# Performance work log

Measured on AMD Instinct MI355X. Metric: run time of the kernel, lower is better.

## Reference

```python
import jax, jax.numpy as jnp
import numpy as np

B, S, D, H = 1, 512, 128, 128
EPS = 1e-5


def layernorm(x, g, b):
    mu = jnp.mean(x, axis=-1, keepdims=True)
    var = jnp.mean(jnp.square(x - mu), axis=-1, keepdims=True)
    return (x - mu) * jax.lax.rsqrt(var + EPS) * g + b


def setup_inputs() -> dict:
    key = jax.random.key(0)
    ks = jax.random.split(key, 10)
    scale_d = 1.0 / np.sqrt(D)
    scale_h = 1.0 / np.sqrt(H)
    return {
        "x": jax.random.normal(ks[0], (B, S, S, D), dtype=jnp.float32),
        "mask": jax.random.uniform(ks[1], (B, S, S), dtype=jnp.float32),
        "norm_g": jnp.ones((D,), jnp.float32),
        "norm_b": jnp.zeros((D,), jnp.float32),
        "Wl": jax.random.normal(ks[2], (H, D), jnp.float32) * scale_d,
        "Wr": jax.random.normal(ks[3], (H, D), jnp.float32) * scale_d,
        "Wlg": jax.random.normal(ks[4], (H, D), jnp.float32) * scale_d,
        "Wrg": jax.random.normal(ks[5], (H, D), jnp.float32) * scale_d,
        "Wog": jax.random.normal(ks[6], (H, D), jnp.float32) * scale_d,
        "out_norm_g": jnp.ones((H,), jnp.float32),
        "out_norm_b": jnp.zeros((H,), jnp.float32),
        "Wout": jax.random.normal(ks[7], (D, H), jnp.float32) * scale_h,
    }


def reference(x, mask, norm_g, norm_b, Wl, Wr, Wlg, Wrg, Wog, out_norm_g, out_norm_b, Wout):
    # x: [B,S,S,D], mask: [B,S,S]
    xn = layernorm(x, norm_g, norm_b)
    m = mask[..., None]  # [B,S,S,1]
    left = (xn @ Wl.T) * m * jax.nn.sigmoid(xn @ Wlg.T)   # [B,S,S,H]
    right = (xn @ Wr.T) * m * jax.nn.sigmoid(xn @ Wrg.T)  # [B,S,S,H]
    out_gate = jax.nn.sigmoid(xn @ Wog.T)                  # [B,S,S,H]
    # per-channel triangular contraction over k
    out = jnp.einsum('bikd,bjkd->bijd', left, right)       # [B,S,S,H]
    out = layernorm(out, out_norm_g, out_norm_b) * out_gate
    return out @ Wout.T  # [B,S,S,D]
```

## Files before the change

kernel.cpp:

```cpp
#include <hip/hip_runtime.h>
#include <hip/hip_bf16.h>
#include <cstdint>

typedef unsigned short u16;
typedef unsigned int   u32;
typedef __bf16 bf16x8 __attribute__((ext_vector_type(8)));
typedef float  f32x4  __attribute__((ext_vector_type(4)));

#define S_    512
#define D_    128
#define H_    128
#define NPOS_ (S_ * S_)
#define LN_EPS 1e-5f

__device__ __forceinline__ u16 f2bf(float f) {
  union { __hip_bfloat16 h; u16 u; } cv;
  cv.h = __float2bfloat16(f);
  return cv.u;
}
__device__ __forceinline__ float bflo(u32 p) { return __uint_as_float(p << 16); }
__device__ __forceinline__ float bfhi(u32 p) { return __uint_as_float(p & 0xffff0000u); }
__device__ __forceinline__ float sigmoidf_(float x) { return 1.f / (1.f + __expf(-x)); }

__device__ __forceinline__ void gld16(const void* g, void* l) {
  __builtin_amdgcn_global_load_lds(
      (const __attribute__((address_space(1))) void*)g,
      (__attribute__((address_space(3))) void*)l, 16, 0, 0);
}

template <int CPR, int TOTAL>
__device__ __forceinline__ void stage_tile(const char* gbase, int ld_bytes, char* lds, int tid) {
#pragma unroll
  for (int c = tid; c < TOTAL; c += 256) {
    int row = c / CPR;
    int col = c - row * CPR;
    gld16(gbase + (size_t)row * ld_bytes + (size_t)col * 16, lds + (size_t)c * 16);
  }
}

__global__ __launch_bounds__(256) void k_prep(
    const float* __restrict__ wl, const float* __restrict__ wlg,
    const float* __restrict__ wr, const float* __restrict__ wrg,
    const float* __restrict__ wog, const float* __restrict__ wout,
    u16* __restrict__ wb) {
  int i = blockIdx.x * 256 + threadIdx.x;
  int m = i >> 14, o = i & 16383;
  const float* src = (m == 0) ? wl : (m == 1) ? wlg : (m == 2) ? wr
                   : (m == 3) ? wrg : (m == 4) ? wog : wout;
  wb[i] = f2bf(src[o]);
}

__global__ __launch_bounds__(256) void k_ln(
    const float* __restrict__ x, const float* __restrict__ ng,
    const float* __restrict__ nb, u32* __restrict__ xn) {
  const int l  = threadIdx.x & 63;
  const int wid = (blockIdx.x * 256 + threadIdx.x) >> 6;
  const int nw  = (gridDim.x * 256) >> 6;
  const float2 gg = ((const float2*)ng)[l];
  const float2 bb = ((const float2*)nb)[l];
  for (int row = wid; row < NPOS_; row += nw) {
    float2 v = ((const float2*)(x + (size_t)row * D_))[l];
    float s = v.x + v.y;
    float q = v.x * v.x + v.y * v.y;
#pragma unroll
    for (int off = 32; off >= 1; off >>= 1) {
      s += __shfl_xor(s, off);
      q += __shfl_xor(q, off);
    }
    float mu  = s * (1.f / 128.f);
    float var = q * (1.f / 128.f) - mu * mu;
    float rs  = rsqrtf(var + LN_EPS);
    float a = (v.x - mu) * rs * gg.x + bb.x;
    float b = (v.y - mu) * rs * gg.y + bb.y;
    xn[(size_t)row * 64 + l] = (u32)f2bf(a) | ((u32)f2bf(b) << 16);
  }
}

__global__ __launch_bounds__(256, 2) void k_proj(
    const u16* __restrict__ xn, const float* __restrict__ mask,
    const u16* __restrict__ wb, u16* __restrict__ left_t,
    u16* __restrict__ right_t, u16* __restrict__ gate_t) {
  __shared__ u16 Bs[128 * 64];
  __shared__ u16 As0[128 * 64];
  __shared__ u16 As1[128 * 64];
  const int g   = blockIdx.y;
  const int r0  = blockIdx.x * 128;
  const int tid = threadIdx.x;
  const int w = tid >> 6, l = tid & 63;
  const int wr = w >> 1, wc = w & 1;
  const u16* W0 = wb + (size_t)((g == 2) ? 4 : 2 * g) * (H_ * D_);
  const u16* W1 = wb + (size_t)(2 * g + 1) * (H_ * D_);

  const f32x4 vz = {0.f, 0.f, 0.f, 0.f};
  f32x4 acc0[4][4], acc1[4][4];
#pragma unroll
  for (int i = 0; i < 4; ++i)
#pragma unroll
    for (int j = 0; j < 4; ++j) { acc0[i][j] = vz; acc1[i][j] = vz; }

#pragma unroll
  for (int kt = 0; kt < 2; ++kt) {
    stage_tile<8, 1024>((const char*)xn + ((size_t)r0 * D_ + kt * 64) * 2, D_ * 2, (char*)Bs, tid);
    stage_tile<8, 1024>((const char*)W0 + (size_t)(kt * 64) * 2, D_ * 2, (char*)As0, tid);
    if (g < 2)
      stage_tile<8, 1024>((const char*)W1 + (size_t)(kt * 64) * 2, D_ * 2, (char*)As1, tid);
    __syncthreads();
#pragma unroll
    for (int kk = 0; kk < 2; ++kk) {
      const int ko = kk * 32 + (l >> 4) * 8;
      bf16x8 bfr[4], a0[4], a1[4];
#pragma unroll
      for (int ni = 0; ni < 4; ++ni)
        bfr[ni] = *(const bf16x8*)&Bs[(wc * 64 + ni * 16 + (l & 15)) * 64 + ko];
#pragma unroll
      for (int mi = 0; mi < 4; ++mi)
        a0[mi] = *(const bf16x8*)&As0[(wr * 64 + mi * 16 + (l & 15)) * 64 + ko];
      if (g < 2) {
#pragma unroll
        for (int mi = 0; mi < 4; ++mi)
          a1[mi] = *(const bf16x8*)&As1[(wr * 64 + mi * 16 + (l & 15)) * 64 + ko];
      }
#pragma unroll
      for (int mi = 0; mi < 4; ++mi)
#pragma unroll
        for (int ni = 0; ni < 4; ++ni) {
          acc0[mi][ni] = __builtin_amdgcn_mfma_f32_16x16x32_bf16(a0[mi], bfr[ni], acc0[mi][ni], 0, 0, 0);
          if (g < 2)
            acc1[mi][ni] = __builtin_amdgcn_mfma_f32_16x16x32_bf16(a1[mi], bfr[ni], acc1[mi][ni], 0, 0, 0);
        }
    }
    __syncthreads();
  }

  const int quad = l >> 4, lc = l & 15;
  u16* dst = (g == 0) ? left_t : (g == 1) ? right_t : gate_t;
#pragma unroll
  for (int ni = 0; ni < 4; ++ni) {
    const int r = r0 + wc * 64 + ni * 16 + lc;
    const float mk = (g < 2) ? mask[r] : 0.f;
#pragma unroll
    for (int mi = 0; mi < 4; ++mi) {
#pragma unroll
      for (int reg = 0; reg < 4; ++reg) {
        const int hrow = wr * 64 + mi * 16 + quad * 4 + reg;
        float v0 = acc0[mi][ni][reg];
        float o;
        if (g < 2) o = v0 * mk * sigmoidf_(acc1[mi][ni][reg]);
        else       o = sigmoidf_(v0);
        dst[(size_t)hrow * NPOS_ + r] = f2bf(o);
      }
    }
  }
}

__global__ __launch_bounds__(256, 2) void k_einsum(
    const u16* __restrict__ left_t, const u16* __restrict__ right_t,
    u16* __restrict__ out_t) {
  const int d = blockIdx.x;
  const int t = blockIdx.y;
  const int i0 = (t >> 2) * 128, j0 = (t & 3) * 128;
  __shared__ u16 As[128 * 64], Bs[128 * 64];
  const u16* L = left_t + (size_t)d * NPOS_;
  const u16* R = right_t + (size_t)d * NPOS_;
  const int tid = threadIdx.x;
  const int w = tid >> 6, l = tid & 63;
  const int wr = w >> 1, wc = w & 1;

  const f32x4 vz = {0.f, 0.f, 0.f, 0.f};
  f32x4 acc[4][4];
#pragma unroll
  for (int i = 0; i < 4; ++i)
#pragma unroll
    for (int j = 0; j < 4; ++j) acc[i][j] = vz;

  for (int kt = 0; kt < 8; ++kt) {
    stage_tile<8, 1024>((const char*)L + ((size_t)i0 * S_ + kt * 64) * 2, S_ * 2, (char*)As, tid);
    stage_tile<8, 1024>((const char*)R + ((size_t)j0 * S_ + kt * 64) * 2, S_ * 2, (char*)Bs, tid);
    __syncthreads();
#pragma unroll
    for (int kk = 0; kk < 2; ++kk) {
      const int ko = kk * 32 + (l >> 4) * 8;
      bf16x8 a[4], b[4];
#pragma unroll
      for (int mi = 0; mi < 4; ++mi)
        a[mi] = *(const bf16x8*)&As[(wr * 64 + mi * 16 + (l & 15)) * 64 + ko];
#pragma unroll
      for (int ni = 0; ni < 4; ++ni)
        b[ni] = *(const bf16x8*)&Bs[(wc * 64 + ni * 16 + (l & 15)) * 64 + ko];
#pragma unroll
      for (int mi = 0; mi < 4; ++mi)
#pragma unroll
        for (int ni = 0; ni < 4; ++ni)
          acc[mi][ni] = __builtin_amdgcn_mfma_f32_16x16x32_bf16(a[mi], b[ni], acc[mi][ni], 0, 0, 0);
    }
    __syncthreads();
  }

  const int quad = l >> 4, lc = l & 15;
  u16* O = out_t + (size_t)d * NPOS_;
#pragma unroll
  for (int mi = 0; mi < 4; ++mi)
#pragma unroll
    for (int ni = 0; ni < 4; ++ni) {
      const int col = j0 + wc * 64 + ni * 16 + lc;
#pragma unroll
      for (int reg = 0; reg < 4; ++reg) {
        const int row = i0 + wr * 64 + mi * 16 + quad * 4 + reg;
        O[(size_t)row * S_ + col] = f2bf(acc[mi][ni][reg]);
      }
    }
}

__global__ __launch_bounds__(256, 2) void k_final(
    const u16* __restrict__ out_t, const u16* __restrict__ gate_t,
    const float* __restrict__ og, const float* __restrict__ ob,
    const u16* __restrict__ wout_b, float* __restrict__ out) {
  __shared__ u16 A_lds[128 * 136];
  __shared__ u16 Wlds[128 * 128];
  __shared__ float psum[4][128], pq[4][128];
  __shared__ float mu_s[128], rs_s[128];
  const int tid = threadIdx.x, w = tid >> 6, l = tid & 63;
  const int r0 = blockIdx.x * 128;

  stage_tile<16, 2048>((const char*)wout_b, 256, (char*)Wlds, tid);

  float s0 = 0.f, s1 = 0.f, q0 = 0.f, q1 = 0.f;
  for (int it = 0; it < 32; ++it) {
    int d = it * 4 + w;
    u32 p = *(const u32*)&out_t[(size_t)d * NPOS_ + r0 + 2 * l];
    float f0 = bflo(p), f1 = bfhi(p);
    s0 += f0; s1 += f1; q0 += f0 * f0; q1 += f1 * f1;
  }
  psum[w][2 * l] = s0; psum[w][2 * l + 1] = s1;
  pq[w][2 * l] = q0;   pq[w][2 * l + 1] = q1;
  __syncthreads();
  if (tid < 128) {
    float s = psum[0][tid] + psum[1][tid] + psum[2][tid] + psum[3][tid];
    float q = pq[0][tid] + pq[1][tid] + pq[2][tid] + pq[3][tid];
    float mu  = s * (1.f / 128.f);
    float var = q * (1.f / 128.f) - mu * mu;
    mu_s[tid] = mu;
    rs_s[tid] = rsqrtf(var + LN_EPS);
  }
  __syncthreads();

  for (int it = 0; it < 32; ++it) {
    int d = it * 4 + w;
    u32 p  = *(const u32*)&out_t[(size_t)d * NPOS_ + r0 + 2 * l];
    u32 gp = *(const u32*)&gate_t[(size_t)d * NPOS_ + r0 + 2 * l];
    float gd = og[d], bd = ob[d];
    float f0 = bflo(p), f1 = bfhi(p);
    float g0 = bflo(gp), g1 = bfhi(gp);
    int ja = 2 * l, jb = 2 * l + 1;
    float a0 = ((f0 - mu_s[ja]) * rs_s[ja] * gd + bd) * g0;
    float a1 = ((f1 - mu_s[jb]) * rs_s[jb] * gd + bd) * g1;
    A_lds[(size_t)ja * 136 + d] = f2bf(a0);
    A_lds[(size_t)jb * 136 + d] = f2bf(a1);
  }
  __syncthreads();

  const int wr = w >> 1, wc = w & 1;
  const f32x4 vz = {0.f, 0.f, 0.f, 0.f};
  f32x4 acc[4][4];
#pragma unroll
  for (int i = 0; i < 4; ++i)
#pragma unroll
    for (int j = 0; j < 4; ++j) acc[i][j] = vz;
#pragma unroll
  for (int kk = 0; kk < 4; ++kk) {
    const int ko = kk * 32 + (l >> 4) * 8;
    bf16x8 a[4], b[4];
#pragma unroll
    for (int mi = 0; mi < 4; ++mi)
      a[mi] = *(const bf16x8*)&A_lds[(wr * 64 + mi * 16 + (l & 15)) * 136 + ko];
#pragma unroll
    for (int ni = 0; ni < 4; ++ni)
      b[ni] = *(const bf16x8*)&Wlds[(wc * 64 + ni * 16 + (l & 15)) * 128 + ko];
#pragma unroll
    for (int mi = 0; mi < 4; ++mi)
#pragma unroll
      for (int ni = 0; ni < 4; ++ni)
        acc[mi][ni] = __builtin_amdgcn_mfma_f32_16x16x32_bf16(a[mi], b[ni], acc[mi][ni], 0, 0, 0);
  }
  const int quad = l >> 4, lc = l & 15;
#pragma unroll
  for (int mi = 0; mi < 4; ++mi)
#pragma unroll
    for (int ni = 0; ni < 4; ++ni) {
      const int dout = wc * 64 + ni * 16 + lc;
#pragma unroll
      for (int reg = 0; reg < 4; ++reg) {
        const int row = r0 + wr * 64 + mi * 16 + quad * 4 + reg;
        out[(size_t)row * D_ + dout] = acc[mi][ni][reg];
      }
    }
}

extern "C" void kernel_launch(void* const* d_in, const int* in_sizes, int n_in,
                              void* d_out, int out_size, void* d_ws, size_t ws_size,
                              hipStream_t stream) {
  const float* x    = (const float*)d_in[0];
  const float* mask = (const float*)d_in[1];
  const float* ng   = (const float*)d_in[2];
  const float* nb   = (const float*)d_in[3];
  const float* Wl   = (const float*)d_in[4];
  const float* Wr   = (const float*)d_in[5];
  const float* Wlg  = (const float*)d_in[6];
  const float* Wrg  = (const float*)d_in[7];
  const float* Wog  = (const float*)d_in[8];
  const float* og   = (const float*)d_in[9];
  const float* ob   = (const float*)d_in[10];
  const float* Wout = (const float*)d_in[11];
  float* out = (float*)d_out;

  const size_t SLAB = (size_t)NPOS_ * H_ * 2;
  char* ws = (char*)d_ws;
  u16* xn      = (u16*)(ws);
  u16* left_t  = (u16*)(ws + SLAB);
  u16* right_t = (u16*)(ws + 2 * SLAB);
  u16* gate_t  = (u16*)(ws + 3 * SLAB);
  u16* wb      = (u16*)(ws + 4 * SLAB);
  u16* out_t   = xn;
  if (ws_size < 4 * SLAB + 6 * H_ * D_ * sizeof(u16)) return;

  k_prep<<<384, 256, 0, stream>>>(Wl, Wlg, Wr, Wrg, Wog, Wout, wb);
  k_ln<<<2048, 256, 0, stream>>>(x, ng, nb, (u32*)xn);
  k_proj<<<dim3(2048, 3), 256, 0, stream>>>(xn, mask, wb, left_t, right_t, gate_t);
  k_einsum<<<dim3(128, 16), 256, 0, stream>>>(left_t, right_t, out_t);
  k_final<<<2048, 256, 0, stream>>>(out_t, gate_t, og, ob, wb + 5 * H_ * D_, out);
}
```

Baseline: 496.8 us.

## Fuse input layernorm into projection kernel with swizzled LDS tile

Merges the layernorm and projection kernels. Each block normalizes its 128 rows straight into an XOR-swizzled LDS tile and then computes all five projections from that tile, instead of three separate blocks each re-reading a bf16 xn buffer. Weight fragments are now read directly from global memory (L2-cached) rather than staged into LDS. This removes the xn round-trip through HBM, one kernel launch, and the triple reload of activations. In exchange each block does more serial work and relies on cached global loads for the weights.

```diff
diff --git a/kernel.cpp b/kernel.cpp
--- a/kernel.cpp
+++ b/kernel.cpp
@@ -50,106 +50,122 @@
   wb[i] = f2bf(src[o]);
 }
 
-__global__ __launch_bounds__(256) void k_ln(
-    const float* __restrict__ x, const float* __restrict__ ng,
-    const float* __restrict__ nb, u32* __restrict__ xn) {
-  const int l  = threadIdx.x & 63;
-  const int wid = (blockIdx.x * 256 + threadIdx.x) >> 6;
-  const int nw  = (gridDim.x * 256) >> 6;
-  const float2 gg = ((const float2*)ng)[l];
-  const float2 bb = ((const float2*)nb)[l];
-  for (int row = wid; row < NPOS_; row += nw) {
-    float2 v = ((const float2*)(x + (size_t)row * D_))[l];
-    float s = v.x + v.y;
-    float q = v.x * v.x + v.y * v.y;
-#pragma unroll
-    for (int off = 32; off >= 1; off >>= 1) {
-      s += __shfl_xor(s, off);
-      q += __shfl_xor(q, off);
-    }
-    float mu  = s * (1.f / 128.f);
-    float var = q * (1.f / 128.f) - mu * mu;
-    float rs  = rsqrtf(var + LN_EPS);
-    float a = (v.x - mu) * rs * gg.x + bb.x;
-    float b = (v.y - mu) * rs * gg.y + bb.y;
-    xn[(size_t)row * 64 + l] = (u32)f2bf(a) | ((u32)f2bf(b) << 16);
-  }
-}
-
-__global__ __launch_bounds__(256, 2) void k_proj(
-    const u16* __restrict__ xn, const float* __restrict__ mask,
+__device__ __forceinline__ void proj_k128(
+    const u16* __restrict__ Wm, const u16* __restrict__ Wg,
+    const u16* Xs, int wr, int wc, int quad, int lq,
+    f32x4 acc0[4][4], f32x4 acc1[4][4]) {
+#pragma unroll
+  for (int ks = 0; ks < 4; ++ks) {
+    const int kc = ks * 4 + quad;
+    bf16x8 b[4], am[4], ag[4];
+#pragma unroll
+    for (int ni = 0; ni < 4; ++ni) {
+      const int br = wc * 64 + ni * 16 + lq;
+      b[ni] = *(const bf16x8*)((const char*)Xs + br * 256 + ((kc ^ (br & 15)) << 4));
+    }
+#pragma unroll
+    for (int mi = 0; mi < 4; ++mi) {
+      const int ar = wr * 64 + mi * 16 + lq;
+      am[mi] = *(const bf16x8*)&Wm[(size_t)ar * D_ + kc * 8];
+      if (Wg) ag[mi] = *(const bf16x8*)&Wg[(size_t)ar * D_ + kc * 8];
+    }
+#pragma unroll
+    for (int mi = 0; mi < 4; ++mi)
+#pragma unroll
+      for (int ni = 0; ni < 4; ++ni) {
+        acc0[mi][ni] = __builtin_amdgcn_mfma_f32_16x16x32_bf16(am[mi], b[ni], acc0[mi][ni], 0, 0, 0);
+        if (Wg)
+          acc1[mi][ni] = __builtin_amdgcn_mfma_f32_16x16x32_bf16(ag[mi], b[ni], acc1[mi][ni], 0, 0, 0);
+      }
+  }
+}
+
+__global__ __launch_bounds__(256, 2) void k_lnproj(
+    const float* __restrict__ x, const float* __restrict__ mask,
+    const float* __restrict__ ng, const float* __restrict__ nb,
     const u16* __restrict__ wb, u16* __restrict__ left_t,
     u16* __restrict__ right_t, u16* __restrict__ gate_t) {
-  __shared__ u16 Bs[128 * 64];
-  __shared__ u16 As0[128 * 64];
-  __shared__ u16 As1[128 * 64];
-  const int g   = blockIdx.y;
-  const int r0  = blockIdx.x * 128;
-  const int tid = threadIdx.x;
-  const int w = tid >> 6, l = tid & 63;
-  const int wr = w >> 1, wc = w & 1;
-  const u16* W0 = wb + (size_t)((g == 2) ? 4 : 2 * g) * (H_ * D_);
-  const u16* W1 = wb + (size_t)(2 * g + 1) * (H_ * D_);
-
+  __shared__ u16 Xs[128 * 128];
+  const int tid = threadIdx.x, w = tid >> 6, l = tid & 63;
+  const int r0 = blockIdx.x * 128;
+  const int half = l >> 5, lh = l & 31;
+
+  {
+    const float4 gg = ((const float4*)ng)[lh];
+    const float4 bb = ((const float4*)nb)[lh];
+#pragma unroll 4
+    for (int it = 0; it < 16; ++it) {
+      const int rr = it * 8 + w * 2 + half;
+      float4 v = ((const float4*)(x + (size_t)(r0 + rr) * D_))[lh];
+      float s = v.x + v.y + v.z + v.w;
+      float q = v.x * v.x + v.y * v.y + v.z * v.z + v.w * v.w;
+#pragma unroll
+      for (int off = 16; off >= 1; off >>= 1) {
+        s += __shfl_xor(s, off);
+        q += __shfl_xor(q, off);
+      }
+      const float mu  = s * (1.f / 128.f);
+      const float var = q * (1.f / 128.f) - mu * mu;
+      const float rs  = rsqrtf(var + LN_EPS);
+      const u32 p0 = (u32)f2bf((v.x - mu) * rs * gg.x + bb.x)
+                   | ((u32)f2bf((v.y - mu) * rs * gg.y + bb.y) << 16);
+      const u32 p1 = (u32)f2bf((v.z - mu) * rs * gg.z + bb.z)
+                   | ((u32)f2bf((v.w - mu) * rs * gg.w + bb.w) << 16);
+      u32* d = (u32*)((char*)Xs + rr * 256 + ((((lh >> 1)) ^ (rr & 15)) << 4) + ((lh & 1) << 3));
+      d[0] = p0;
+      d[1] = p1;
+    }
+  }
+  __syncthreads();
+
+  const int wr = w >> 1, wc = w & 1, quad = l >> 4, lq = l & 15;
   const f32x4 vz = {0.f, 0.f, 0.f, 0.f};
   f32x4 acc0[4][4], acc1[4][4];
+
+#pragma unroll
+  for (int g = 0; g < 2; ++g) {
+    const u16* Wm = wb + (size_t)(2 * g) * (H_ * D_);
+    const u16* Wg = wb + (size_t)(2 * g + 1) * (H_ * D_);
+    u16* dst = g ? right_t : left_t;
+#pragma unroll
+    for (int i = 0; i < 4; ++i)
+#pragma unroll
+      for (int j = 0; j < 4; ++j) { acc0[i][j] = vz; acc1[i][j] = vz; }
+
+    proj_k128(Wm, Wg, Xs, wr, wc, quad, lq, acc0, acc1);
+
+#pragma unroll
+    for (int ni = 0; ni < 4; ++ni) {
+      const int r = r0 + wc * 64 + ni * 16 + lq;
+      const float mk = mask[r];
+#pragma unroll
+      for (int mi = 0; mi < 4; ++mi)
+#pragma unroll
+        for (int reg = 0; reg < 4; ++reg) {
+          const int hrow = wr * 64 + mi * 16 + quad * 4 + reg;
+          dst[(size_t)hrow * NPOS_ + r] =
+              f2bf(acc0[mi][ni][reg] * mk * sigmoidf_(acc1[mi][ni][reg]));
+        }
+    }
+  }
+
 #pragma unroll
   for (int i = 0; i < 4; ++i)
 #pragma unroll
-    for (int j = 0; j < 4; ++j) { acc0[i][j] = vz; acc1[i][j] = vz; }
-
-#pragma unroll
-  for (int kt = 0; kt < 2; ++kt) {
-    stage_tile<8, 1024>((const char*)xn + ((size_t)r0 * D_ + kt * 64) * 2, D_ * 2, (char*)Bs, tid);
-    stage_tile<8, 1024>((const char*)W0 + (size_t)(kt * 64) * 2, D_ * 2, (char*)As0, tid);
-    if (g < 2)
-      stage_tile<8, 1024>((const char*)W1 + (size_t)(kt * 64) * 2, D_ * 2, (char*)As1, tid);
-    __syncthreads();
-#pragma unroll
-    for (int kk = 0; kk < 2; ++kk) {
-      const int ko = kk * 32 + (l >> 4) * 8;
-      bf16x8 bfr[4], a0[4], a1[4];
-#pragma unroll
-      for (int ni = 0; ni < 4; ++ni)
-        bfr[ni] = *(const bf16x8*)&Bs[(wc * 64 + ni * 16 + (l & 15)) * 64 + ko];
-#pragma unroll
-      for (int mi = 0; mi < 4; ++mi)
-        a0[mi] = *(const bf16x8*)&As0[(wr * 64 + mi * 16 + (l & 15)) * 64 + ko];
-      if (g < 2) {
-#pragma unroll
-        for (int mi = 0; mi < 4; ++mi)
-          a1[mi] = *(const bf16x8*)&As1[(wr * 64 + mi * 16 + (l & 15)) * 64 + ko];
-      }
-#pragma unroll
-      for (int mi = 0; mi < 4; ++mi)
-#pragma unroll
-        for (int ni = 0; ni < 4; ++ni) {
-          acc0[mi][ni] = __builtin_amdgcn_mfma_f32_16x16x32_bf16(a0[mi], bfr[ni], acc0[mi][ni], 0, 0, 0);
-          if (g < 2)
-            acc1[mi][ni] = __builtin_amdgcn_mfma_f32_16x16x32_bf16(a1[mi], bfr[ni], acc1[mi][ni], 0, 0, 0);
-        }
-    }
-    __syncthreads();
-  }
-
-  const int quad = l >> 4, lc = l & 15;
-  u16* dst = (g == 0) ? left_t : (g == 1) ? right_t : gate_t;
+    for (int j = 0; j < 4; ++j) acc0[i][j] = vz;
+
+  proj_k128(wb + (size_t)4 * (H_ * D_), (const u16*)nullptr, Xs, wr, wc, quad, lq, acc0, acc1);
+
 #pragma unroll
   for (int ni = 0; ni < 4; ++ni) {
-    const int r = r0 + wc * 64 + ni * 16 + lc;
-    const float mk = (g < 2) ? mask[r] : 0.f;
-#pragma unroll
-    for (int mi = 0; mi < 4; ++mi) {
+    const int r = r0 + wc * 64 + ni * 16 + lq;
+#pragma unroll
+    for (int mi = 0; mi < 4; ++mi)
 #pragma unroll
       for (int reg = 0; reg < 4; ++reg) {
         const int hrow = wr * 64 + mi * 16 + quad * 4 + reg;
-        float v0 = acc0[mi][ni][reg];
-        float o;
-        if (g < 2) o = v0 * mk * sigmoidf_(acc1[mi][ni][reg]);
-        else       o = sigmoidf_(v0);
-        dst[(size_t)hrow * NPOS_ + r] = f2bf(o);
-      }
-    }
+        gate_t[(size_t)hrow * NPOS_ + r] = f2bf(sigmoidf_(acc0[mi][ni][reg]));
+      }
   }
 }
 
@@ -315,17 +331,15 @@
 
   const size_t SLAB = (size_t)NPOS_ * H_ * 2;
   char* ws = (char*)d_ws;
-  u16* xn      = (u16*)(ws);
   u16* left_t  = (u16*)(ws + SLAB);
   u16* right_t = (u16*)(ws + 2 * SLAB);
   u16* gate_t  = (u16*)(ws + 3 * SLAB);
   u16* wb      = (u16*)(ws + 4 * SLAB);
-  u16* out_t   = xn;
+  u16* out_t   = (u16*)(ws);
   if (ws_size < 4 * SLAB + 6 * H_ * D_ * sizeof(u16)) return;
 
   k_prep<<<384, 256, 0, stream>>>(Wl, Wlg, Wr, Wrg, Wog, Wout, wb);
-  k_ln<<<2048, 256, 0, stream>>>(x, ng, nb, (u32*)xn);
-  k_proj<<<dim3(2048, 3), 256, 0, stream>>>(xn, mask, wb, left_t, right_t, gate_t);
+  k_lnproj<<<2048, 256, 0, stream>>>(x, mask, ng, nb, wb, left_t, right_t, gate_t);
   k_einsum<<<dim3(128, 16), 256, 0, stream>>>(left_t, right_t, out_t);
   k_final<<<2048, 256, 0, stream>>>(out_t, gate_t, og, ob, wb + 5 * H_ * D_, out);
 }
```

Measured after the change: 476.0 us. 4.2% less time.
